# Kernel tuning notes

Hardware: AMD Instinct MI355X
Metric: run time of the kernel (lower is better)

The kernel has to match this reference:

```python
import jax, jax.numpy as jnp
import numpy as np

DX = 1.0
DY = 1.0
W_DIV = 1e9
W_SMOOTH = 10.0
W_STD = 100.0
EPS = 1e-10


def _corner(a, i, j, k):
    # slice dims 2,3,4: 0 -> [0:-1], 1 -> [1:]
    sl = lambda b: slice(1, None) if b else slice(0, -1)
    return a[:, :, sl(i), sl(j), sl(k)]


def setup_inputs() -> dict:
    key = jax.random.key(0)
    k1, k2 = jax.random.split(key)
    outputs = jax.random.normal(k1, (2, 1, 256, 256, 64), dtype=jnp.float32)
    targets = jax.random.normal(k2, (2, 3, 256, 256, 64), dtype=jnp.float32)
    return {"outputs": outputs, "targets": targets}


def _loss(outputs, targets):
    bx, by, bz = targets[:, 0:1], targets[:, 1:2], targets[:, 2:3]
    z = outputs[:, 0:1]

    # vertical thickness and smoothness of its square
    dz = z[..., 1:] - z[..., :-1]
    dz2 = dz ** 2
    lap = (6 * dz2[:, :, 1:-1, 1:-1, 1:-1]
           - dz2[:, :, :-2, 1:-1, 1:-1] - dz2[:, :, 2:, 1:-1, 1:-1]
           - dz2[:, :, 1:-1, :-2, 1:-1] - dz2[:, :, 1:-1, 2:, 1:-1]
           - dz2[:, :, 1:-1, 1:-1, 2:] - dz2[:, :, 1:-1, 1:-1, :-2])
    loss_smooth = jnp.mean(lap ** 2)

    # per-(batch, channel, z) std over the spatial plane (unbiased, matching torch.std)
    loss_std = jnp.mean(jnp.std(dz, axis=(2, 3), ddof=1))

    # 8 cell corners for each field
    corners = lambda a: {(i, j, k): _corner(a, i, j, k)
                         for i in (0, 1) for j in (0, 1) for k in (0, 1)}
    BX, BY, BZ, Z = corners(bx), corners(by), corners(bz), corners(z)

    az = lambda a, b: jnp.abs(Z[a] - Z[b])
    num = (0.25 * (BX[1,0,0] + BX[1,1,0] + BX[1,0,1] + BX[1,1,1]) * DY * 0.5 * (az((1,0,1),(1,0,0)) + az((1,1,1),(1,1,0)))
           - 0.25 * (BX[0,0,0] + BX[0,1,0] + BX[0,0,1] + BX[0,1,1]) * DY * 0.5 * (az((0,0,1),(0,0,0)) + az((0,1,1),(0,1,0)))
           + 0.25 * (BY[0,1,0] + BY[1,1,0] + BY[0,1,1] + BY[1,1,1]) * DX * 0.5 * (az((0,1,1),(0,1,0)) + az((1,1,1),(1,1,0)))
           - 0.25 * (BY[0,0,0] + BY[1,0,0] + BY[0,0,1] + BY[1,0,1]) * DX * 0.5 * (az((0,0,1),(0,0,0)) + az((1,0,1),(1,0,0)))
           + 0.25 * (BZ[0,0,1] + BZ[0,1,1] + BZ[1,0,1] + BZ[1,1,1]) * DX * DY
           - 0.25 * (BZ[0,0,0] + BZ[0,1,0] + BZ[1,0,0] + BZ[1,1,0]) * DX * DY
           + (BX[0,0,1] + BX[1,0,1] + BX[1,1,1]) * DY * (Z[0,0,1] - Z[1,0,1]) / 6
           + (BX[0,1,1] + BX[1,1,1] + BX[1,0,1]) * DY * (Z[0,1,1] - Z[1,1,1]) / 6
           + (BY[1,0,1] + BY[1,1,1] + BY[0,1,1]) * DX * (Z[1,0,1] - Z[1,1,1]) / 6
           + (BY[0,0,1] + BY[0,1,1] + BY[1,1,1]) * DX * (Z[0,0,1] - Z[0,1,1]) / 6
           - (BX[0,0,0] + BX[1,0,0] + BX[1,1,0]) * DY * (Z[0,0,0] - Z[1,0,0]) / 6
           - (BX[0,1,0] + BX[1,1,0] + BX[1,0,0]) * DY * (Z[0,1,0] - Z[1,1,0]) / 6
           - (BY[1,0,0] + BY[1,1,0] + BY[0,1,0]) * DX * (Z[1,0,0] - Z[1,1,0]) / 6
           - (BY[0,0,0] + BY[0,1,0] + BY[1,1,0]) * DX * (Z[0,0,0] - Z[0,1,0]) / 6)

    sum8 = lambda C: sum(C.values())
    den = ((sum8(BX) * 0.125) ** 2 + (sum8(BY) * 0.125) ** 2
           + (sum8(BZ) * 0.125) ** 2 + EPS)
    loss_div = jnp.mean(num ** 2 / den)

    return loss_div * W_DIV, loss_smooth * W_SMOOTH + loss_std * W_STD


def reference(outputs, targets):
    return _loss(outputs, targets)
```

## Files before the change

kernel.cpp:

```cpp
#include <hip/hip_runtime.h>
#include <math.h>


__global__ __launch_bounds__(512) void zero_ws_kernel(float* ws) {
    for (int i = threadIdx.x; i < 32 * 258; i += 512) ws[i] = 0.0f;
}

__device__ __forceinline__ void ld5(float* a, const float* p, int d4) {
    float4 x = *(const float4*)p;
    float4 y = *(const float4*)(p + d4);
    a[0] = x.x; a[1] = x.y; a[2] = x.z; a[3] = x.w; a[4] = y.x;
}

__global__ __launch_bounds__(256, 4) void fused_loss_kernel(
    const float* __restrict__ zin, const float* __restrict__ tg,
    float* __restrict__ ws)
{
    __shared__ float r1[1024];
    __shared__ float r2[1024];
    __shared__ float rsc[4][2];

    const int tid  = threadIdx.x;
    const int lane = tid & 63;
    const int w    = tid >> 6;

    const int bb   = blockIdx.x >> 12;
    const int rest = blockIdx.x & 4095;
    const int x0 = ((rest >> 6) & 63) << 2;
    const int y0 = (rest & 63) << 2;

    const int c  = tid >> 4;
    const int kq = tid & 15;
    const int cx = c & 3, cy = c >> 2;
    const int xg = x0 + cx, yg = y0 + cy;
    const int k0 = kq << 2;
    const int d4 = (kq < 15) ? 4 : 0;

    const int xE = (xg < 255) ? xg + 1 : 255;
    const int xW = (xg > 0)   ? xg - 1 : 0;
    const int yN = (yg < 255) ? yg + 1 : 255;
    const int yS = (yg > 0)   ? yg - 1 : 0;

    const int oC  = xg * 16384 + yg * 64 + k0;
    const int oE  = xE * 16384 + yg * 64 + k0;
    const int oW  = xW * 16384 + yg * 64 + k0;
    const int oN  = xg * 16384 + yN * 64 + k0;
    const int oS  = xg * 16384 + yS * 64 + k0;
    const int oNE = xE * 16384 + yN * 64 + k0;

    const float* zg = zin + ((size_t)bb << 22);

    float zcv[7];
    {
        int km = (k0 >= 4) ? -4 : 0;
        float4 m = *(const float4*)&zg[oC + km];
        float4 a = *(const float4*)&zg[oC];
        float4 b = *(const float4*)&zg[oC + d4];
        zcv[0] = m.w; zcv[1] = a.x; zcv[2] = a.y; zcv[3] = a.z; zcv[4] = a.w;
        zcv[5] = b.x; zcv[6] = b.y;
    }
    float zEv[5], zWv[5], zNv[5], zSv[5], zNEv[5];
    ld5(zEv,  &zg[oE],  d4);
    ld5(zWv,  &zg[oW],  d4);
    ld5(zNv,  &zg[oN],  d4);
    ld5(zSv,  &zg[oS],  d4);
    ld5(zNEv, &zg[oNE], d4);

    float dz0[4], dzE[4], dzN[4], dzNE[4];
    #pragma unroll
    for (int e = 0; e < 4; ++e) {
        dz0[e]  = zcv[e + 2] - zcv[e + 1];
        dzE[e]  = zEv[e + 1] - zEv[e];
        dzN[e]  = zNv[e + 1] - zNv[e];
        dzNE[e] = zNEv[e + 1] - zNEv[e];
    }
    float s1a[4], s2a[4];
    #pragma unroll
    for (int e = 0; e < 4; ++e) {
        bool kok = (k0 + e) < 63;
        s1a[e] = kok ? dz0[e] : 0.0f;
        s2a[e] = kok ? dz0[e] * dz0[e] : 0.0f;
    }

    float sm = 0.0f;
    if (xg >= 1 && xg <= 254 && yg >= 1 && yg <= 254) {
        #pragma unroll
        for (int e = 0; e < 4; ++e) {
            int k = k0 + e;
            if (k >= 1 && k <= 61) {
                float dzm = zcv[e + 1] - zcv[e];
                float dzp = zcv[e + 3] - zcv[e + 2];
                float dzw = zWv[e + 1] - zWv[e];
                float dzs = zSv[e + 1] - zSv[e];
                float lap = 6.0f * dz0[e] * dz0[e]
                          - dzw * dzw - dzE[e] * dzE[e]
                          - dzs * dzs - dzN[e] * dzN[e]
                          - dzm * dzm - dzp * dzp;
                sm += lap * lap;
            }
        }
    }

    float dv = 0.0f;
    if (xg < 255 && yg < 255) {
        float dCE[5], dCN[5], dENE[5], dNNE[5];
        #pragma unroll
        for (int j = 0; j < 5; ++j) {
            dCE[j]  = zcv[j + 1] - zEv[j];
            dCN[j]  = zcv[j + 1] - zNv[j];
            dENE[j] = zEv[j] - zNEv[j];
            dNNE[j] = zNv[j] - zNEv[j];
        }
        float adz00[4], adz10[4], adz01[4], adz11[4];
        #pragma unroll
        for (int e = 0; e < 4; ++e) {
            adz00[e] = fabsf(dz0[e]);  adz10[e] = fabsf(dzE[e]);
            adz01[e] = fabsf(dzN[e]);  adz11[e] = fabsf(dzNE[e]);
        }

        const int p00 = oC, p10 = oE, p01 = oN, p11 = oNE;
        const float* bxg = tg + ((size_t)(bb * 3) << 22);
        const float* byg = bxg + (1u << 22);
        const float* bzg = byg + (1u << 22);
        const float c6 = 1.0f / 6.0f;

        float num[4], den[4];

        {
            float a00[5], a10[5], a01[5], a11[5];
            ld5(a00, &bxg[p00], d4);  ld5(a10, &bxg[p10], d4);
            ld5(a01, &bxg[p01], d4);  ld5(a11, &bxg[p11], d4);
            #pragma unroll
            for (int e = 0; e < 4; ++e) {
                float s10 = a10[e] + a10[e + 1] + a11[e] + a11[e + 1];
                float s00 = a00[e] + a00[e + 1] + a01[e] + a01[e + 1];
                num[e] = 0.125f * (s10 * (adz10[e] + adz11[e])
                                 - s00 * (adz00[e] + adz01[e]));
                num[e] += c6 * ( (a00[e + 1] + a10[e + 1] + a11[e + 1]) * dCE[e + 1]
                               + (a01[e + 1] + a11[e + 1] + a10[e + 1]) * dNNE[e + 1]
                               - (a00[e] + a10[e] + a11[e]) * dCE[e]
                               - (a01[e] + a11[e] + a10[e]) * dNNE[e] );
                float sbx = s10 + s00;
                den[e] = sbx * sbx;
            }
        }
        {
            float a00[5], a10[5], a01[5], a11[5];
            ld5(a00, &byg[p00], d4);  ld5(a10, &byg[p10], d4);
            ld5(a01, &byg[p01], d4);  ld5(a11, &byg[p11], d4);
            #pragma unroll
            for (int e = 0; e < 4; ++e) {
                float s01 = a01[e] + a01[e + 1] + a11[e] + a11[e + 1];
                float s00 = a00[e] + a00[e + 1] + a10[e] + a10[e + 1];
                num[e] += 0.125f * (s01 * (adz01[e] + adz11[e])
                                  - s00 * (adz00[e] + adz10[e]));
                num[e] += c6 * ( (a10[e + 1] + a11[e + 1] + a01[e + 1]) * dENE[e + 1]
                               + (a00[e + 1] + a01[e + 1] + a11[e + 1]) * dCN[e + 1]
                               - (a10[e] + a11[e] + a01[e]) * dENE[e]
                               - (a00[e] + a01[e] + a11[e]) * dCN[e] );
                float sby = s01 + s00;
                den[e] += sby * sby;
            }
        }
        {
            float a00[5], a10[5], a01[5], a11[5];
            ld5(a00, &bzg[p00], d4);  ld5(a10, &bzg[p10], d4);
            ld5(a01, &bzg[p01], d4);  ld5(a11, &bzg[p11], d4);
            #pragma unroll
            for (int e = 0; e < 4; ++e) {
                float slo = a00[e] + a10[e] + a01[e] + a11[e];
                float shi = a00[e + 1] + a10[e + 1] + a01[e + 1] + a11[e + 1];
                num[e] += 0.25f * (shi - slo);
                float sbz = slo + shi;
                den[e] += sbz * sbz;
            }
        }
        #pragma unroll
        for (int e = 0; e < 4; ++e) {
            if ((k0 + e) < 63) {
                float d = den[e] * 0.015625f + 1e-10f;
                dv += num[e] * num[e] * __builtin_amdgcn_rcpf(d);
            }
        }
    }

    #pragma unroll
    for (int off = 32; off > 0; off >>= 1) {
        sm += __shfl_down(sm, off, 64);
        dv += __shfl_down(dv, off, 64);
    }

    { float4 v; v.x = s1a[0]; v.y = s1a[1]; v.z = s1a[2]; v.w = s1a[3];
      *(float4*)&r1[tid << 2] = v; }
    { float4 v; v.x = s2a[0]; v.y = s2a[1]; v.z = s2a[2]; v.w = s2a[3];
      *(float4*)&r2[tid << 2] = v; }
    if (lane == 0) { rsc[w][0] = sm; rsc[w][1] = dv; }
    __syncthreads();

    if (tid < 64) {
        float a = 0.0f, b2 = 0.0f;
        #pragma unroll
        for (int cc = 0; cc < 16; ++cc) {
            a  += r1[cc * 64 + tid];
            b2 += r2[cc * 64 + tid];
        }
        float* sl = ws + (blockIdx.x & 31) * 258;
        if (tid < 63) {
            atomicAdd(&sl[2 + bb * 64 + tid],   a);
            atomicAdd(&sl[130 + bb * 64 + tid], b2);
        }
        if (tid == 0) atomicAdd(&sl[0], rsc[0][0] + rsc[1][0] + rsc[2][0] + rsc[3][0]);
        if (tid == 1) atomicAdd(&sl[1], rsc[0][1] + rsc[1][1] + rsc[2][1] + rsc[3][1]);
    }
}

__global__ __launch_bounds__(128) void finalize_kernel(const float* __restrict__ ws,
                                                       float* __restrict__ out)
{
    __shared__ double red[128];
    const int t = threadIdx.x;
    double stdv = 0.0;
    {
        int k = t & 63, bb = t >> 6;
        if (k < 63) {
            double s1 = 0.0, s2 = 0.0;
            for (int p = 0; p < 32; ++p) {
                s1 += (double)ws[p * 258 + 2 + bb * 64 + k];
                s2 += (double)ws[p * 258 + 130 + bb * 64 + k];
            }
            const double N = 65536.0;
            double var = (s2 - s1 * s1 / N) / (N - 1.0);
            stdv = sqrt(var > 0.0 ? var : 0.0);
        }
    }
    red[t] = stdv;
    __syncthreads();
    for (int off = 64; off > 0; off >>= 1) {
        if (t < off) red[t] += red[t + off];
        __syncthreads();
    }
    if (t == 0) {
        double smt = 0.0, dvt = 0.0;
        for (int p = 0; p < 32; ++p) {
            smt += (double)ws[p * 258 + 0];
            dvt += (double)ws[p * 258 + 1];
        }
        double loss_std    = red[0] / 126.0;
        double loss_smooth = smt / (2.0 * 254.0 * 254.0 * 61.0);
        double loss_div    = dvt / (2.0 * 255.0 * 255.0 * 63.0);
        out[0] = (float)(loss_div * 1e9);
        out[1] = (float)(loss_smooth * 10.0 + loss_std * 100.0);
    }
}

extern "C" void kernel_launch(void* const* d_in, const int* in_sizes, int n_in,
                              void* d_out, int out_size, void* d_ws, size_t ws_size,
                              hipStream_t stream) {
    const float* z  = (const float*)d_in[0];
    const float* tg = (const float*)d_in[1];
    float* out = (float*)d_out;
    float* ws  = (float*)d_ws;

    zero_ws_kernel<<<1, 512, 0, stream>>>(ws);
    fused_loss_kernel<<<8192, 256, 0, stream>>>(z, tg, ws);
    finalize_kernel<<<1, 128, 0, stream>>>(ws, out);
}
```

Before: 210.9 us.

## Stage B-field tile with halo in LDS and remap block order for XCD locality

Each block now cooperatively loads a 5x5x64 tile (including halo) of the three B-field components into shared memory. The per-thread corner loads then read from LDS instead of issuing four overlapping global loads per field. The block index is also remapped so that consecutive blocks on the same XCD cover neighbouring spatial tiles, and the reduction scratch buffers reuse the staging LDS. This removes redundant global/L2 traffic but adds an extra barrier and raises LDS use per block, which may affect occupancy.

New measurement: 206.9 us. About the same (-1.9%).

```diff
diff --git a/kernel.cpp b/kernel.cpp
--- a/kernel.cpp
+++ b/kernel.cpp
@@ -1,6 +1,9 @@
 #include <hip/hip_runtime.h>
 #include <math.h>
 
+
+#define BSTR 324
+#define BFLD 1620
 
 __global__ __launch_bounds__(512) void zero_ws_kernel(float* ws) {
     for (int i = threadIdx.x; i < 32 * 258; i += 512) ws[i] = 0.0f;
@@ -16,18 +19,32 @@
     const float* __restrict__ zin, const float* __restrict__ tg,
     float* __restrict__ ws)
 {
-    __shared__ float r1[1024];
-    __shared__ float r2[1024];
+    __shared__ float bs[3 * BFLD];
     __shared__ float rsc[4][2];
 
     const int tid  = threadIdx.x;
     const int lane = tid & 63;
     const int w    = tid >> 6;
 
-    const int bb   = blockIdx.x >> 12;
-    const int rest = blockIdx.x & 4095;
+    const int virt = ((blockIdx.x & 7) << 10) | (blockIdx.x >> 3);
+    const int bb   = virt >> 12;
+    const int rest = virt & 4095;
     const int x0 = ((rest >> 6) & 63) << 2;
     const int y0 = (rest & 63) << 2;
+
+    for (int i = tid; i < 1200; i += 256) {
+        int f  = i / 400;
+        int jj = i - f * 400;
+        int row = jj >> 4;
+        int o   = (jj & 15) << 2;
+        int xi  = row / 5;
+        int yr  = row - xi * 5;
+        int x = x0 + xi; x = x > 255 ? 255 : x;
+        int y = y0 + yr; y = y > 255 ? 255 : y;
+        const float* g = tg + ((size_t)(bb * 3 + f) << 22);
+        *(float4*)&bs[f * BFLD + xi * BSTR + yr * 64 + o] =
+            *(const float4*)&g[x * 16384 + y * 64 + o];
+    }
 
     const int c  = tid >> 4;
     const int kq = tid & 15;
@@ -101,6 +118,8 @@
         }
     }
 
+    __syncthreads();
+
     float dv = 0.0f;
     if (xg < 255 && yg < 255) {
         float dCE[5], dCN[5], dENE[5], dNNE[5];
@@ -118,18 +137,17 @@
             adz01[e] = fabsf(dzN[e]);  adz11[e] = fabsf(dzNE[e]);
         }
 
-        const int p00 = oC, p10 = oE, p01 = oN, p11 = oNE;
-        const float* bxg = tg + ((size_t)(bb * 3) << 22);
-        const float* byg = bxg + (1u << 22);
-        const float* bzg = byg + (1u << 22);
+        const float* bxP = &bs[cx * BSTR + cy * 64 + k0];
+        const float* byP = bxP + BFLD;
+        const float* bzP = byP + BFLD;
         const float c6 = 1.0f / 6.0f;
 
         float num[4], den[4];
 
         {
             float a00[5], a10[5], a01[5], a11[5];
-            ld5(a00, &bxg[p00], d4);  ld5(a10, &bxg[p10], d4);
-            ld5(a01, &bxg[p01], d4);  ld5(a11, &bxg[p11], d4);
+            ld5(a00, bxP, d4);            ld5(a10, bxP + BSTR, d4);
+            ld5(a01, bxP + 64, d4);       ld5(a11, bxP + BSTR + 64, d4);
             #pragma unroll
             for (int e = 0; e < 4; ++e) {
                 float s10 = a10[e] + a10[e + 1] + a11[e] + a11[e + 1];
@@ -146,8 +164,8 @@
         }
         {
             float a00[5], a10[5], a01[5], a11[5];
-            ld5(a00, &byg[p00], d4);  ld5(a10, &byg[p10], d4);
-            ld5(a01, &byg[p01], d4);  ld5(a11, &byg[p11], d4);
+            ld5(a00, byP, d4);            ld5(a10, byP + BSTR, d4);
+            ld5(a01, byP + 64, d4);       ld5(a11, byP + BSTR + 64, d4);
             #pragma unroll
             for (int e = 0; e < 4; ++e) {
                 float s01 = a01[e] + a01[e + 1] + a11[e] + a11[e + 1];
@@ -164,8 +182,8 @@
         }
         {
             float a00[5], a10[5], a01[5], a11[5];
-            ld5(a00, &bzg[p00], d4);  ld5(a10, &bzg[p10], d4);
-            ld5(a01, &bzg[p01], d4);  ld5(a11, &bzg[p11], d4);
+            ld5(a00, bzP, d4);            ld5(a10, bzP + BSTR, d4);
+            ld5(a01, bzP + 64, d4);       ld5(a11, bzP + BSTR + 64, d4);
             #pragma unroll
             for (int e = 0; e < 4; ++e) {
                 float slo = a00[e] + a10[e] + a01[e] + a11[e];
@@ -190,6 +208,9 @@
         dv += __shfl_down(dv, off, 64);
     }
 
+    __syncthreads();
+    float* r1 = bs;
+    float* r2 = bs + 1024;
     { float4 v; v.x = s1a[0]; v.y = s1a[1]; v.z = s1a[2]; v.w = s1a[3];
       *(float4*)&r1[tid << 2] = v; }
     { float4 v; v.x = s2a[0]; v.y = s2a[1]; v.z = s2a[2]; v.w = s2a[3];
```

## Hoist target loads ahead of compute, interleave block order, factor divergence algebra

Applied to the files above, without the earlier changes.

All 24 target-field vector loads are issued up front, unconditionally, next to the z loads, so more memory requests are in flight. Interior tiles get a fast path that builds neighbour offsets by simple addition instead of clamped index maths. Block indices are permuted so consecutive blocks land in different regions, and the divergence terms are rewritten to share partial sums across the k window. Launch bounds drop to 3 blocks per SM to leave room for the extra live registers, at the cost of occupancy and of loads now also made for edge cells that previously skipped them.

After: 216.1 us. 1.02x slower.

```diff
diff --git a/kernel.cpp b/kernel.cpp
--- a/kernel.cpp
+++ b/kernel.cpp
@@ -1,6 +1,8 @@
 #include <hip/hip_runtime.h>
 #include <math.h>
 
+
+#define XSF 16384
 
 __global__ __launch_bounds__(512) void zero_ws_kernel(float* ws) {
     for (int i = threadIdx.x; i < 32 * 258; i += 512) ws[i] = 0.0f;
@@ -12,7 +14,7 @@
     a[0] = x.x; a[1] = x.y; a[2] = x.z; a[3] = x.w; a[4] = y.x;
 }
 
-__global__ __launch_bounds__(256, 4) void fused_loss_kernel(
+__global__ __launch_bounds__(256, 3) void fused_loss_kernel(
     const float* __restrict__ zin, const float* __restrict__ tg,
     float* __restrict__ ws)
 {
@@ -24,8 +26,9 @@
     const int lane = tid & 63;
     const int w    = tid >> 6;
 
-    const int bb   = blockIdx.x >> 12;
-    const int rest = blockIdx.x & 4095;
+    const int virt = ((blockIdx.x & 7) << 10) | (blockIdx.x >> 3);
+    const int bb   = virt >> 12;
+    const int rest = virt & 4095;
     const int x0 = ((rest >> 6) & 63) << 2;
     const int y0 = (rest & 63) << 2;
 
@@ -34,21 +37,31 @@
     const int cx = c & 3, cy = c >> 2;
     const int xg = x0 + cx, yg = y0 + cy;
     const int k0 = kq << 2;
-    const int d4 = (kq < 15) ? 4 : 0;
-
-    const int xE = (xg < 255) ? xg + 1 : 255;
-    const int xW = (xg > 0)   ? xg - 1 : 0;
-    const int yN = (yg < 255) ? yg + 1 : 255;
-    const int yS = (yg > 0)   ? yg - 1 : 0;
-
-    const int oC  = xg * 16384 + yg * 64 + k0;
-    const int oE  = xE * 16384 + yg * 64 + k0;
-    const int oW  = xW * 16384 + yg * 64 + k0;
-    const int oN  = xg * 16384 + yN * 64 + k0;
-    const int oS  = xg * 16384 + yS * 64 + k0;
-    const int oNE = xE * 16384 + yN * 64 + k0;
-
-    const float* zg = zin + ((size_t)bb << 22);
+
+    const bool interior = (x0 >= 4) && (x0 <= 248) && (y0 >= 4) && (y0 <= 248);
+
+    const int oC = xg * XSF + yg * 64 + k0;
+    int oE, oW, oN, oS, oNE, d4;
+    if (interior) {
+        oE = oC + XSF; oW = oC - XSF; oN = oC + 64; oS = oC - 64; oNE = oC + XSF + 64;
+        d4 = 4;
+    } else {
+        const int xE = (xg < 255) ? xg + 1 : 255;
+        const int xW = (xg > 0)   ? xg - 1 : 0;
+        const int yN = (yg < 255) ? yg + 1 : 255;
+        const int yS = (yg > 0)   ? yg - 1 : 0;
+        oE  = xE * XSF + yg * 64 + k0;
+        oW  = xW * XSF + yg * 64 + k0;
+        oN  = xg * XSF + yN * 64 + k0;
+        oS  = xg * XSF + yS * 64 + k0;
+        oNE = xE * XSF + yN * 64 + k0;
+        d4  = (kq < 15) ? 4 : 0;
+    }
+
+    const float* zg  = zin + ((size_t)bb << 22);
+    const float* bxg = tg  + ((size_t)(bb * 3) << 22);
+    const float* byg = bxg + (1u << 22);
+    const float* bzg = byg + (1u << 22);
 
     float zcv[7];
     {
@@ -65,6 +78,16 @@
     ld5(zNv,  &zg[oN],  d4);
     ld5(zSv,  &zg[oS],  d4);
     ld5(zNEv, &zg[oNE], d4);
+
+    float X00[5], X10[5], X01[5], X11[5];
+    ld5(X00, &bxg[oC], d4);  ld5(X10, &bxg[oE], d4);
+    ld5(X01, &bxg[oN], d4);  ld5(X11, &bxg[oNE], d4);
+    float Y00[5], Y10[5], Y01[5], Y11[5];
+    ld5(Y00, &byg[oC], d4);  ld5(Y10, &byg[oE], d4);
+    ld5(Y01, &byg[oN], d4);  ld5(Y11, &byg[oNE], d4);
+    float Z00[5], Z10[5], Z01[5], Z11[5];
+    ld5(Z00, &bzg[oC], d4);  ld5(Z10, &bzg[oE], d4);
+    ld5(Z01, &bzg[oN], d4);  ld5(Z11, &bzg[oNE], d4);
 
     float dz0[4], dzE[4], dzN[4], dzNE[4];
     #pragma unroll
@@ -111,68 +134,60 @@
             dENE[j] = zEv[j] - zNEv[j];
             dNNE[j] = zNv[j] - zNEv[j];
         }
-        float adz00[4], adz10[4], adz01[4], adz11[4];
+        float sxp[4], sxm[4], syp[4], sym[4];
         #pragma unroll
         for (int e = 0; e < 4; ++e) {
-            adz00[e] = fabsf(dz0[e]);  adz10[e] = fabsf(dzE[e]);
-            adz01[e] = fabsf(dzN[e]);  adz11[e] = fabsf(dzNE[e]);
-        }
-
-        const int p00 = oC, p10 = oE, p01 = oN, p11 = oNE;
-        const float* bxg = tg + ((size_t)(bb * 3) << 22);
-        const float* byg = bxg + (1u << 22);
-        const float* bzg = byg + (1u << 22);
+            float aC = fabsf(dz0[e]),  aE  = fabsf(dzE[e]);
+            float aN = fabsf(dzN[e]),  aNE = fabsf(dzNE[e]);
+            sxp[e] = aE + aNE;  sxm[e] = aC + aN;
+            syp[e] = aN + aNE;  sym[e] = aC + aE;
+        }
+
         const float c6 = 1.0f / 6.0f;
-
         float num[4], den[4];
 
         {
-            float a00[5], a10[5], a01[5], a11[5];
-            ld5(a00, &bxg[p00], d4);  ld5(a10, &bxg[p10], d4);
-            ld5(a01, &bxg[p01], d4);  ld5(a11, &bxg[p11], d4);
+            float qx[5], px2[5], g[5];
+            #pragma unroll
+            for (int j = 0; j < 5; ++j) {
+                qx[j]  = X10[j] + X11[j];
+                px2[j] = X00[j] + X01[j];
+                g[j]   = (qx[j] + X00[j]) * dCE[j] + (qx[j] + X01[j]) * dNNE[j];
+            }
             #pragma unroll
             for (int e = 0; e < 4; ++e) {
-                float s10 = a10[e] + a10[e + 1] + a11[e] + a11[e + 1];
-                float s00 = a00[e] + a00[e + 1] + a01[e] + a01[e + 1];
-                num[e] = 0.125f * (s10 * (adz10[e] + adz11[e])
-                                 - s00 * (adz00[e] + adz01[e]));
-                num[e] += c6 * ( (a00[e + 1] + a10[e + 1] + a11[e + 1]) * dCE[e + 1]
-                               + (a01[e + 1] + a11[e + 1] + a10[e + 1]) * dNNE[e + 1]
-                               - (a00[e] + a10[e] + a11[e]) * dCE[e]
-                               - (a01[e] + a11[e] + a10[e]) * dNNE[e] );
-                float sbx = s10 + s00;
-                den[e] = sbx * sbx;
+                float qq = qx[e] + qx[e + 1], pp = px2[e] + px2[e + 1];
+                num[e] = 0.125f * (qq * sxp[e] - pp * sxm[e]) + c6 * (g[e + 1] - g[e]);
+                float s = qq + pp;
+                den[e] = s * s;
             }
         }
         {
-            float a00[5], a10[5], a01[5], a11[5];
-            ld5(a00, &byg[p00], d4);  ld5(a10, &byg[p10], d4);
-            ld5(a01, &byg[p01], d4);  ld5(a11, &byg[p11], d4);
+            float qy[5], py2[5], h[5];
+            #pragma unroll
+            for (int j = 0; j < 5; ++j) {
+                qy[j]  = Y01[j] + Y11[j];
+                py2[j] = Y00[j] + Y10[j];
+                h[j]   = (qy[j] + Y10[j]) * dENE[j] + (qy[j] + Y00[j]) * dCN[j];
+            }
             #pragma unroll
             for (int e = 0; e < 4; ++e) {
-                float s01 = a01[e] + a01[e + 1] + a11[e] + a11[e + 1];
-                float s00 = a00[e] + a00[e + 1] + a10[e] + a10[e + 1];
-                num[e] += 0.125f * (s01 * (adz01[e] + adz11[e])
-                                  - s00 * (adz00[e] + adz10[e]));
-                num[e] += c6 * ( (a10[e + 1] + a11[e + 1] + a01[e + 1]) * dENE[e + 1]
-                               + (a00[e + 1] + a01[e + 1] + a11[e + 1]) * dCN[e + 1]
-                               - (a10[e] + a11[e] + a01[e]) * dENE[e]
-                               - (a00[e] + a01[e] + a11[e]) * dCN[e] );
-                float sby = s01 + s00;
-                den[e] += sby * sby;
+                float qq = qy[e] + qy[e + 1], pp = py2[e] + py2[e + 1];
+                num[e] += 0.125f * (qq * syp[e] - pp * sym[e]) + c6 * (h[e + 1] - h[e]);
+                float s = qq + pp;
+                den[e] += s * s;
             }
         }
         {
-            float a00[5], a10[5], a01[5], a11[5];
-            ld5(a00, &bzg[p00], d4);  ld5(a10, &bzg[p10], d4);
-            ld5(a01, &bzg[p01], d4);  ld5(a11, &bzg[p11], d4);
+            float sz[5];
+            #pragma unroll
+            for (int j = 0; j < 5; ++j)
+                sz[j] = Z00[j] + Z10[j] + Z01[j] + Z11[j];
             #pragma unroll
             for (int e = 0; e < 4; ++e) {
-                float slo = a00[e] + a10[e] + a01[e] + a11[e];
-                float shi = a00[e + 1] + a10[e + 1] + a01[e + 1] + a11[e + 1];
-                num[e] += 0.25f * (shi - slo);
-                float sbz = slo + shi;
-                den[e] += sbz * sbz;
+                num[e] += 0.25f * (sz[e + 1] - sz[e]);
+                float s = sz[e] + sz[e + 1];
+                den[e] += s * s;
             }
         }
         #pragma unroll
```
